# Kernel tuning notes

Hardware: AMD Instinct MI355X
Metric: run time of the kernel (lower is better)

Reference implementation:

```python
import jax, jax.numpy as jnp
import numpy as np

B, H = 1024, 1024
V_OUT, V_INP = 50000, 32000
SRC = 256


def setup_inputs() -> dict:
    key = jax.random.key(0)
    ks = jax.random.split(key, 8)
    x = jax.random.normal(ks[0], (B, H), dtype=jnp.float32)
    W = jax.random.normal(ks[1], (V_OUT, H), dtype=jnp.float32) * 0.02
    b = jax.random.normal(ks[2], (V_OUT,), dtype=jnp.float32) * 0.02
    attn_scores = jax.random.uniform(ks[3], (B, SRC), dtype=jnp.float32)
    ctx_ids = jax.random.randint(ks[4], (B, SRC), 0, V_INP)
    inp_to_act = jax.random.randint(ks[5], (V_INP,), 0, V_OUT)
    out_map = jax.random.randint(ks[6], (V_OUT,), 0, V_OUT)
    actionmask = jax.random.randint(ks[7], (B, V_OUT), 0, 2).astype(jnp.int32)
    return {"x": x, "W": W, "b": b, "attn_scores": attn_scores,
            "ctx_ids": ctx_ids, "inp_to_act": inp_to_act,
            "out_map": out_map, "actionmask": actionmask}


def reference(x, W, b, attn_scores, ctx_ids, inp_to_act, out_map, actionmask):
    # gen scores: dense projection to output vocab, then remap rare ids
    gen_scores = x @ W.T + b                      # [B, V_out]
    gen_scores = gen_scores[:, out_map]           # index_select along vocab

    # pointer distribution: scatter-add attention mass onto input vocab ids
    bsz = gen_scores.shape[0]
    inpdist = jnp.zeros((bsz, V_INP), dtype=gen_scores.dtype)
    inpdist = inpdist.at[jnp.arange(bsz)[:, None], ctx_ids].add(attn_scores)

    # map input-vocab mass onto output vocab ids (scatter/set)
    ptr_scores = jnp.zeros((bsz, V_OUT), dtype=gen_scores.dtype)
    ptr_scores = ptr_scores.at[:, inp_to_act].set(inpdist)

    out_scores = gen_scores + ptr_scores
    gen_masked = gen_scores + (-1e6) * actionmask.astype(gen_scores.dtype)
    out_probs = jax.nn.softmax(out_scores, axis=-1)
    return (out_probs, gen_masked)
```

## Files before the change

kernel.cpp:

```cpp
#include <hip/hip_runtime.h>
#include <hip/hip_bf16.h>

#define B_    1024
#define H_    1024
#define VOUT  50000
#define VINP  32000
#define SRC_  256

#define BM 128
#define BN 128
#define BKK 32

typedef __bf16 bf16x8 __attribute__((ext_vector_type(8)));
typedef __bf16 bf16x4 __attribute__((ext_vector_type(4)));
typedef float  f32x4  __attribute__((ext_vector_type(4)));

__global__ void init_kernel(int* __restrict__ src_inp,
                            float* __restrict__ rowsum)
{
    int i = blockIdx.x * blockDim.x + threadIdx.x;
    if (i < VOUT) src_inp[i] = -1;
    if (i < B_)  rowsum[i] = 0.0f;
}

__global__ void scat_max_kernel(const int* __restrict__ i2a, int* __restrict__ src_inp) {
    int v = blockIdx.x * blockDim.x + threadIdx.x;
    if (v < VINP) atomicMax(&src_inp[i2a[v]], v);
}

__global__ __launch_bounds__(256) void gemm_kernel(
    const float* __restrict__ x, const float* __restrict__ W,
    const float* __restrict__ bias, const int* __restrict__ out_map,
    const int* __restrict__ amask,
    float* __restrict__ out_scores, float* __restrict__ gen_masked,
    float* __restrict__ rowsum)
{
    __shared__ __bf16 As[BM * BKK];
    __shared__ __bf16 Bs[BN * BKK];

    const int id = (int)(blockIdx.x + (blockIdx.y << 3));
    const int g  = id >> 3;
    const int by = (id & 7) * 49 + (g >> 3);
    if (by >= 391) return;
    const int bx = g & 7;
    const int m0 = bx * BM;
    const int n0 = by * BN;

    const int t  = threadIdx.x;
    const int tr = t >> 3;
    const int tk = (t & 7) << 2;

    const float* xrow[4];
    const float* wrow[4];
    #pragma unroll
    for (int p = 0; p < 4; ++p) {
        int r = tr + p * 32;
        xrow[p] = x + (size_t)(m0 + r) * H_ + tk;
        int n = n0 + r; if (n >= VOUT) n = VOUT - 1;
        wrow[p] = W + (size_t)out_map[n] * H_ + tk;
    }

    f32x4 acc[4][4];
    #pragma unroll
    for (int i = 0; i < 4; ++i)
        #pragma unroll
        for (int j = 0; j < 4; ++j)
            acc[i][j] = (f32x4){0.f, 0.f, 0.f, 0.f};

    const int wv   = t >> 6;
    const int wm   = (wv >> 1) * 64;
    const int wn   = (wv & 1) * 64;
    const int lane = t & 63;
    const int quad = lane >> 4;
    const int lr   = lane & 15;

    float4 ar[4], br[4];
    #pragma unroll
    for (int p = 0; p < 4; ++p) {
        ar[p] = *(const float4*)(xrow[p]);
        br[p] = *(const float4*)(wrow[p]);
    }

    for (int k0 = 0; k0 < H_; k0 += BKK) {
        #pragma unroll
        for (int p = 0; p < 4; ++p) {
            int r = tr + p * 32;
            bf16x4 a4, b4;
            a4.x = (__bf16)ar[p].x; a4.y = (__bf16)ar[p].y; a4.z = (__bf16)ar[p].z; a4.w = (__bf16)ar[p].w;
            b4.x = (__bf16)br[p].x; b4.y = (__bf16)br[p].y; b4.z = (__bf16)br[p].z; b4.w = (__bf16)br[p].w;
            *(bf16x4*)(&As[r * BKK + tk]) = a4;
            *(bf16x4*)(&Bs[r * BKK + tk]) = b4;
        }
        __syncthreads();

        if (k0 + BKK < H_) {
            #pragma unroll
            for (int p = 0; p < 4; ++p) {
                ar[p] = *(const float4*)(xrow[p] + k0 + BKK);
                br[p] = *(const float4*)(wrow[p] + k0 + BKK);
            }
        }

        bf16x8 af[4], bfr[4];
        #pragma unroll
        for (int i = 0; i < 4; ++i) {
            af[i]  = *(const bf16x8*)(&As[(wm + i * 16 + lr) * BKK + quad * 8]);
            bfr[i] = *(const bf16x8*)(&Bs[(wn + i * 16 + lr) * BKK + quad * 8]);
        }
        #pragma unroll
        for (int mi = 0; mi < 4; ++mi)
            #pragma unroll
            for (int ni = 0; ni < 4; ++ni)
                acc[mi][ni] = __builtin_amdgcn_mfma_f32_16x16x32_bf16(bfr[ni], af[mi], acc[mi][ni], 0, 0, 0);
        __syncthreads();
    }

    #pragma unroll
    for (int mi = 0; mi < 4; ++mi) {
        const int m = m0 + wm + mi * 16 + lr;
        float psum = 0.0f;
        #pragma unroll
        for (int ni = 0; ni < 4; ++ni) {
            const int n = n0 + wn + ni * 16 + (quad << 2);
            if (n < VOUT) {
                const size_t off = (size_t)m * VOUT + n;
                float4 v;
                v.x = acc[mi][ni][0] + bias[out_map[n + 0]];
                v.y = acc[mi][ni][1] + bias[out_map[n + 1]];
                v.z = acc[mi][ni][2] + bias[out_map[n + 2]];
                v.w = acc[mi][ni][3] + bias[out_map[n + 3]];
                *(float4*)(out_scores + off) = v;
                const int4 am = *(const int4*)(amask + off);
                float4 gm;
                gm.x = v.x - 1000000.0f * (float)am.x;
                gm.y = v.y - 1000000.0f * (float)am.y;
                gm.z = v.z - 1000000.0f * (float)am.z;
                gm.w = v.w - 1000000.0f * (float)am.w;
                *(float4*)(gen_masked + off) = gm;
                psum += __expf(v.x) + __expf(v.y) + __expf(v.z) + __expf(v.w);
            }
        }
        psum += __shfl_xor(psum, 16, 64);
        psum += __shfl_xor(psum, 32, 64);
        if (quad == 0) atomicAdd(rowsum + m, psum);
    }
}

__global__ void ptr_scatter_kernel(const float* __restrict__ attn,
                                   const int* __restrict__ ctx,
                                   const int* __restrict__ i2a,
                                   const int* __restrict__ src_inp,
                                   float* __restrict__ out_scores,
                                   float* __restrict__ rowsum)
{
    int idx = blockIdx.x * blockDim.x + threadIdx.x;
    int i = idx >> 8;
    int v = ctx[idx];
    int o = i2a[v];
    if (src_inp[o] == v) {
        float a   = attn[idx];
        float old = atomicAdd(out_scores + (size_t)i * VOUT + o, a);
        atomicAdd(rowsum + i, __expf(old + a) - __expf(old));
    }
}

__global__ __launch_bounds__(256) void norm_kernel(float* __restrict__ probs,
                                                   const float* __restrict__ rowsum)
{
    const int row = blockIdx.x;
    const float inv = 1.0f / rowsum[row];
    float4* p4 = (float4*)(probs + (size_t)row * VOUT);
    const int base = blockIdx.y * 3125;
    for (int i = base + threadIdx.x; i < base + 3125; i += 256) {
        float4 v = p4[i];
        v.x = __expf(v.x) * inv;
        v.y = __expf(v.y) * inv;
        v.z = __expf(v.z) * inv;
        v.w = __expf(v.w) * inv;
        p4[i] = v;
    }
}

extern "C" void kernel_launch(void* const* d_in, const int* in_sizes, int n_in,
                              void* d_out, int out_size, void* d_ws, size_t ws_size,
                              hipStream_t stream)
{
    const float* x     = (const float*)d_in[0];
    const float* W     = (const float*)d_in[1];
    const float* b     = (const float*)d_in[2];
    const float* attn  = (const float*)d_in[3];
    const int*   ctx   = (const int*)d_in[4];
    const int*   i2a   = (const int*)d_in[5];
    const int*   omap  = (const int*)d_in[6];
    const int*   amask = (const int*)d_in[7];

    float* out_probs  = (float*)d_out;
    float* gen_masked = out_probs + (size_t)B_ * VOUT;

    int*   src_inp = (int*)d_ws;
    float* rowsum  = (float*)(src_inp + VOUT);

    init_kernel<<<(VOUT + 255) / 256, 256, 0, stream>>>(src_inp, rowsum);
    scat_max_kernel<<<(VINP + 255) / 256, 256, 0, stream>>>(i2a, src_inp);

    dim3 grid(B_ / BM, 392);
    gemm_kernel<<<grid, 256, 0, stream>>>(x, W, b, omap, amask,
                                          out_probs, gen_masked, rowsum);

    ptr_scatter_kernel<<<(B_ * SRC_) / 256, 256, 0, stream>>>(attn, ctx, i2a, src_inp,
                                                              out_probs, rowsum);

    norm_kernel<<<dim3(B_, 4), 256, 0, stream>>>(out_probs, rowsum);
}
```

Baseline: 1.170 ms.

## Double-buffer GEMM shared memory and XOR-swizzle LDS layout

The GEMM main loop now uses two LDS buffers and keeps two register prefetch sets, so global loads run two k-steps ahead. This removes one barrier per k-step. The LDS write and read addresses are XOR-swizzled by row to cut bank conflicts on the bf16x8 fragment reads. In exchange it doubles LDS use and adds register pressure from the extra prefetch set, which may lower occupancy.

```diff
diff --git a/kernel.cpp b/kernel.cpp
--- a/kernel.cpp
+++ b/kernel.cpp
@@ -35,8 +35,8 @@
     float* __restrict__ out_scores, float* __restrict__ gen_masked,
     float* __restrict__ rowsum)
 {
-    __shared__ __bf16 As[BM * BKK];
-    __shared__ __bf16 Bs[BN * BKK];
+    __shared__ __bf16 As[2][BM * BKK];
+    __shared__ __bf16 Bs[2][BN * BKK];
 
     const int id = (int)(blockIdx.x + (blockIdx.y << 3));
     const int g  = id >> 3;
@@ -48,16 +48,20 @@
 
     const int t  = threadIdx.x;
     const int tr = t >> 3;
-    const int tk = (t & 7) << 2;
+    const int u  = t & 7;
+    const int tk = u << 2;
 
     const float* xrow[4];
     const float* wrow[4];
+    int scol[4];
     #pragma unroll
     for (int p = 0; p < 4; ++p) {
         int r = tr + p * 32;
         xrow[p] = x + (size_t)(m0 + r) * H_ + tk;
         int n = n0 + r; if (n >= VOUT) n = VOUT - 1;
         wrow[p] = W + (size_t)out_map[n] * H_ + tk;
+        int gg = (r >> 1) & 3;
+        scol[p] = r * BKK + ((((u >> 1) ^ gg) << 3) | ((u & 1) << 2));
     }
 
     f32x4 acc[4][4];
@@ -74,45 +78,64 @@
     const int quad = lane >> 4;
     const int lr   = lane & 15;
 
-    float4 ar[4], br[4];
-    #pragma unroll
-    for (int p = 0; p < 4; ++p) {
-        ar[p] = *(const float4*)(xrow[p]);
-        br[p] = *(const float4*)(wrow[p]);
-    }
-
-    for (int k0 = 0; k0 < H_; k0 += BKK) {
+    auto stage = [&](int buf, const float4* a, const float4* b) {
         #pragma unroll
         for (int p = 0; p < 4; ++p) {
-            int r = tr + p * 32;
             bf16x4 a4, b4;
-            a4.x = (__bf16)ar[p].x; a4.y = (__bf16)ar[p].y; a4.z = (__bf16)ar[p].z; a4.w = (__bf16)ar[p].w;
-            b4.x = (__bf16)br[p].x; b4.y = (__bf16)br[p].y; b4.z = (__bf16)br[p].z; b4.w = (__bf16)br[p].w;
-            *(bf16x4*)(&As[r * BKK + tk]) = a4;
-            *(bf16x4*)(&Bs[r * BKK + tk]) = b4;
-        }
-        __syncthreads();
-
-        if (k0 + BKK < H_) {
-            #pragma unroll
-            for (int p = 0; p < 4; ++p) {
-                ar[p] = *(const float4*)(xrow[p] + k0 + BKK);
-                br[p] = *(const float4*)(wrow[p] + k0 + BKK);
-            }
-        }
-
+            a4.x = (__bf16)a[p].x; a4.y = (__bf16)a[p].y; a4.z = (__bf16)a[p].z; a4.w = (__bf16)a[p].w;
+            b4.x = (__bf16)b[p].x; b4.y = (__bf16)b[p].y; b4.z = (__bf16)b[p].z; b4.w = (__bf16)b[p].w;
+            *(bf16x4*)(&As[buf][scol[p]]) = a4;
+            *(bf16x4*)(&Bs[buf][scol[p]]) = b4;
+        }
+    };
+
+    auto compute = [&](int buf) {
         bf16x8 af[4], bfr[4];
         #pragma unroll
         for (int i = 0; i < 4; ++i) {
-            af[i]  = *(const bf16x8*)(&As[(wm + i * 16 + lr) * BKK + quad * 8]);
-            bfr[i] = *(const bf16x8*)(&Bs[(wn + i * 16 + lr) * BKK + quad * 8]);
+            int Ra = wm + i * 16 + lr;
+            int Rb = wn + i * 16 + lr;
+            af[i]  = *(const bf16x8*)(&As[buf][Ra * BKK + ((quad ^ ((Ra >> 1) & 3)) << 3)]);
+            bfr[i] = *(const bf16x8*)(&Bs[buf][Rb * BKK + ((quad ^ ((Rb >> 1) & 3)) << 3)]);
         }
         #pragma unroll
         for (int mi = 0; mi < 4; ++mi)
             #pragma unroll
             for (int ni = 0; ni < 4; ++ni)
                 acc[mi][ni] = __builtin_amdgcn_mfma_f32_16x16x32_bf16(bfr[ni], af[mi], acc[mi][ni], 0, 0, 0);
+    };
+
+    float4 a0[4], b0[4], a1[4], b1[4];
+    #pragma unroll
+    for (int p = 0; p < 4; ++p) {
+        a0[p] = *(const float4*)(xrow[p]);
+        b0[p] = *(const float4*)(wrow[p]);
+        a1[p] = *(const float4*)(xrow[p] + BKK);
+        b1[p] = *(const float4*)(wrow[p] + BKK);
+    }
+
+    for (int k0 = 0; k0 < H_; k0 += 2 * BKK) {
+        stage(0, a0, b0);
+        if (k0 + 2 * BKK < H_) {
+            #pragma unroll
+            for (int p = 0; p < 4; ++p) {
+                a0[p] = *(const float4*)(xrow[p] + k0 + 2 * BKK);
+                b0[p] = *(const float4*)(wrow[p] + k0 + 2 * BKK);
+            }
+        }
         __syncthreads();
+        compute(0);
+
+        stage(1, a1, b1);
+        if (k0 + 3 * BKK < H_) {
+            #pragma unroll
+            for (int p = 0; p < 4; ++p) {
+                a1[p] = *(const float4*)(xrow[p] + k0 + 3 * BKK);
+                b1[p] = *(const float4*)(wrow[p] + k0 + 3 * BKK);
+            }
+        }
+        __syncthreads();
+        compute(1);
     }
 
     #pragma unroll
```

New measurement: 1.141 ms. 1.03x faster.

## Pre-convert W and x to swizzled bf16 and stage via direct global-to-LDS loads

Applied to the files above, without the earlier changes.

Adds pre-pass kernels that gather W rows through out_map, convert W and x to bf16 in an XOR-swizzled layout, and precompute the remapped bias. The GEMM then uses global_load_lds with double-buffered LDS tiles instead of register fp32 loads plus in-loop conversion, which removes conversion work and the out_map indirection from the main loop and halves operand bytes. This adds a full extra pass over W (about 200MB read, 100MB written) and needs workspace; when workspace is small it borrows the gen_masked buffer and runs a separate mask kernel afterwards.

```diff
diff --git a/kernel.cpp b/kernel.cpp
--- a/kernel.cpp
+++ b/kernel.cpp
@@ -6,14 +6,21 @@
 #define VOUT  50000
 #define VINP  32000
 #define SRC_  256
+#define NPAD  50048
 
 #define BM 128
 #define BN 128
 #define BKK 32
+#define NSTEP (H_ / BKK)
 
 typedef __bf16 bf16x8 __attribute__((ext_vector_type(8)));
-typedef __bf16 bf16x4 __attribute__((ext_vector_type(4)));
 typedef float  f32x4  __attribute__((ext_vector_type(4)));
+
+__device__ __forceinline__ void ldsload16(const __bf16* g, __bf16* l) {
+    __builtin_amdgcn_global_load_lds(
+        (const __attribute__((address_space(1))) void*)g,
+        (__attribute__((address_space(3))) void*)l, 16, 0, 0);
+}
 
 __global__ void init_kernel(int* __restrict__ src_inp,
                             float* __restrict__ rowsum)
@@ -28,15 +35,58 @@
     if (v < VINP) atomicMax(&src_inp[i2a[v]], v);
 }
 
+__global__ __launch_bounds__(256) void conv_w(
+    const float* __restrict__ W, const int* __restrict__ omap,
+    const float* __restrict__ bias,
+    __bf16* __restrict__ wbf, float* __restrict__ bias_g)
+{
+    int idx = blockIdx.x * 256 + threadIdx.x;
+    int n   = idx >> 7;
+    int c7  = idx & 127;
+    bf16x8 v;
+    if (n < VOUT) {
+        int g = (n >> 1) & 3;
+        int chunk = c7 >> 2, w = c7 & 3;
+        const float* s = W + (size_t)omap[n] * H_ + chunk * 32 + ((w ^ g) << 3);
+        float4 f0 = *(const float4*)(s);
+        float4 f1 = *(const float4*)(s + 4);
+        v[0] = (__bf16)f0.x; v[1] = (__bf16)f0.y; v[2] = (__bf16)f0.z; v[3] = (__bf16)f0.w;
+        v[4] = (__bf16)f1.x; v[5] = (__bf16)f1.y; v[6] = (__bf16)f1.z; v[7] = (__bf16)f1.w;
+        if (c7 == 0) bias_g[n] = bias[omap[n]];
+    } else {
+        #pragma unroll
+        for (int e = 0; e < 8; ++e) v[e] = (__bf16)0.f;
+        if (c7 == 0) bias_g[n] = 0.f;
+    }
+    *(bf16x8*)(wbf + (size_t)idx * 8) = v;
+}
+
+__global__ __launch_bounds__(256) void conv_x(
+    const float* __restrict__ x, __bf16* __restrict__ xbf)
+{
+    int idx = blockIdx.x * 256 + threadIdx.x;
+    int m   = idx >> 7;
+    int c7  = idx & 127;
+    int g = (m >> 1) & 3;
+    int chunk = c7 >> 2, w = c7 & 3;
+    const float* s = x + (size_t)m * H_ + chunk * 32 + ((w ^ g) << 3);
+    float4 f0 = *(const float4*)(s);
+    float4 f1 = *(const float4*)(s + 4);
+    bf16x8 v;
+    v[0] = (__bf16)f0.x; v[1] = (__bf16)f0.y; v[2] = (__bf16)f0.z; v[3] = (__bf16)f0.w;
+    v[4] = (__bf16)f1.x; v[5] = (__bf16)f1.y; v[6] = (__bf16)f1.z; v[7] = (__bf16)f1.w;
+    *(bf16x8*)(xbf + (size_t)idx * 8) = v;
+}
+
+template<bool FUSED>
 __global__ __launch_bounds__(256) void gemm_kernel(
-    const float* __restrict__ x, const float* __restrict__ W,
-    const float* __restrict__ bias, const int* __restrict__ out_map,
-    const int* __restrict__ amask,
+    const __bf16* __restrict__ xbf, const __bf16* __restrict__ wbf,
+    const float* __restrict__ bias_g, const int* __restrict__ amask,
     float* __restrict__ out_scores, float* __restrict__ gen_masked,
     float* __restrict__ rowsum)
 {
-    __shared__ __bf16 As[BM * BKK];
-    __shared__ __bf16 Bs[BN * BKK];
+    __shared__ __bf16 As[2][BM * BKK];
+    __shared__ __bf16 Bs[2][BN * BKK];
 
     const int id = (int)(blockIdx.x + (blockIdx.y << 3));
     const int g  = id >> 3;
@@ -46,19 +96,25 @@
     const int m0 = bx * BM;
     const int n0 = by * BN;
 
-    const int t  = threadIdx.x;
-    const int tr = t >> 3;
-    const int tk = (t & 7) << 2;
-
-    const float* xrow[4];
-    const float* wrow[4];
-    #pragma unroll
-    for (int p = 0; p < 4; ++p) {
-        int r = tr + p * 32;
-        xrow[p] = x + (size_t)(m0 + r) * H_ + tk;
-        int n = n0 + r; if (n >= VOUT) n = VOUT - 1;
-        wrow[p] = W + (size_t)out_map[n] * H_ + tk;
-    }
+    const int t    = threadIdx.x;
+    const int wv   = t >> 6;
+    const int lane = t & 63;
+    const int quad = lane >> 4;
+    const int lr   = lane & 15;
+    const int wm   = (wv >> 1) * 64;
+    const int wn   = (wv & 1) * 64;
+
+    const __bf16* gA = xbf + (size_t)(m0 + wv * 16 + (lane >> 2)) * H_ + ((lane & 3) << 3);
+    const __bf16* gB = wbf + (size_t)(n0 + wv * 16 + (lane >> 2)) * H_ + ((lane & 3) << 3);
+
+    auto stage = [&](int buf, int k) {
+        __bf16* a = &As[0][0] + buf * (BM * BKK) + (wv * 16) * BKK;
+        __bf16* b = &Bs[0][0] + buf * (BN * BKK) + (wv * 16) * BKK;
+        ldsload16(gA + k,            a);
+        ldsload16(gA + 64 * H_ + k,  a + 64 * BKK);
+        ldsload16(gB + k,            b);
+        ldsload16(gB + 64 * H_ + k,  b + 64 * BKK);
+    };
 
     f32x4 acc[4][4];
     #pragma unroll
@@ -67,51 +123,30 @@
         for (int j = 0; j < 4; ++j)
             acc[i][j] = (f32x4){0.f, 0.f, 0.f, 0.f};
 
-    const int wv   = t >> 6;
-    const int wm   = (wv >> 1) * 64;
-    const int wn   = (wv & 1) * 64;
-    const int lane = t & 63;
-    const int quad = lane >> 4;
-    const int lr   = lane & 15;
-
-    float4 ar[4], br[4];
-    #pragma unroll
-    for (int p = 0; p < 4; ++p) {
-        ar[p] = *(const float4*)(xrow[p]);
-        br[p] = *(const float4*)(wrow[p]);
-    }
-
-    for (int k0 = 0; k0 < H_; k0 += BKK) {
-        #pragma unroll
-        for (int p = 0; p < 4; ++p) {
-            int r = tr + p * 32;
-            bf16x4 a4, b4;
-            a4.x = (__bf16)ar[p].x; a4.y = (__bf16)ar[p].y; a4.z = (__bf16)ar[p].z; a4.w = (__bf16)ar[p].w;
-            b4.x = (__bf16)br[p].x; b4.y = (__bf16)br[p].y; b4.z = (__bf16)br[p].z; b4.w = (__bf16)br[p].w;
-            *(bf16x4*)(&As[r * BKK + tk]) = a4;
-            *(bf16x4*)(&Bs[r * BKK + tk]) = b4;
-        }
-        __syncthreads();
-
-        if (k0 + BKK < H_) {
-            #pragma unroll
-            for (int p = 0; p < 4; ++p) {
-                ar[p] = *(const float4*)(xrow[p] + k0 + BKK);
-                br[p] = *(const float4*)(wrow[p] + k0 + BKK);
-            }
-        }
-
+    auto compute = [&](int buf) {
+        const __bf16* a  = &As[0][0] + buf * (BM * BKK);
+        const __bf16* bp = &Bs[0][0] + buf * (BN * BKK);
         bf16x8 af[4], bfr[4];
         #pragma unroll
         for (int i = 0; i < 4; ++i) {
-            af[i]  = *(const bf16x8*)(&As[(wm + i * 16 + lr) * BKK + quad * 8]);
-            bfr[i] = *(const bf16x8*)(&Bs[(wn + i * 16 + lr) * BKK + quad * 8]);
+            int Ra = wm + i * 16 + lr;
+            int Rb = wn + i * 16 + lr;
+            af[i]  = *(const bf16x8*)(a  + Ra * BKK + ((quad ^ ((Ra >> 1) & 3)) << 3));
+            bfr[i] = *(const bf16x8*)(bp + Rb * BKK + ((quad ^ ((Rb >> 1) & 3)) << 3));
         }
         #pragma unroll
         for (int mi = 0; mi < 4; ++mi)
             #pragma unroll
             for (int ni = 0; ni < 4; ++ni)
                 acc[mi][ni] = __builtin_amdgcn_mfma_f32_16x16x32_bf16(bfr[ni], af[mi], acc[mi][ni], 0, 0, 0);
+    };
+
+    stage(0, 0);
+    __syncthreads();
+    for (int ts = 0; ts < NSTEP; ++ts) {
+        int cur = ts & 1;
+        if (ts + 1 < NSTEP) stage(cur ^ 1, (ts + 1) * BKK);
+        compute(cur);
         __syncthreads();
     }
 
@@ -124,19 +159,22 @@
             const int n = n0 + wn + ni * 16 + (quad << 2);
             if (n < VOUT) {
                 const size_t off = (size_t)m * VOUT + n;
+                const float4 bb = *(const float4*)(bias_g + n);
                 float4 v;
-                v.x = acc[mi][ni][0] + bias[out_map[n + 0]];
-                v.y = acc[mi][ni][1] + bias[out_map[n + 1]];
-                v.z = acc[mi][ni][2] + bias[out_map[n + 2]];
-                v.w = acc[mi][ni][3] + bias[out_map[n + 3]];
+                v.x = acc[mi][ni][0] + bb.x;
+                v.y = acc[mi][ni][1] + bb.y;
+                v.z = acc[mi][ni][2] + bb.z;
+                v.w = acc[mi][ni][3] + bb.w;
                 *(float4*)(out_scores + off) = v;
-                const int4 am = *(const int4*)(amask + off);
-                float4 gm;
-                gm.x = v.x - 1000000.0f * (float)am.x;
-                gm.y = v.y - 1000000.0f * (float)am.y;
-                gm.z = v.z - 1000000.0f * (float)am.z;
-                gm.w = v.w - 1000000.0f * (float)am.w;
-                *(float4*)(gen_masked + off) = gm;
+                if (FUSED) {
+                    const int4 am = *(const int4*)(amask + off);
+                    float4 gm;
+                    gm.x = v.x - 1000000.0f * (float)am.x;
+                    gm.y = v.y - 1000000.0f * (float)am.y;
+                    gm.z = v.z - 1000000.0f * (float)am.z;
+                    gm.w = v.w - 1000000.0f * (float)am.w;
+                    *(float4*)(gen_masked + off) = gm;
+                }
                 psum += __expf(v.x) + __expf(v.y) + __expf(v.z) + __expf(v.w);
             }
         }
@@ -144,6 +182,21 @@
         psum += __shfl_xor(psum, 32, 64);
         if (quad == 0) atomicAdd(rowsum + m, psum);
     }
+}
+
+__global__ __launch_bounds__(256) void mask_kernel(
+    const float* __restrict__ scores, const int* __restrict__ amask,
+    float* __restrict__ gen)
+{
+    size_t i = (size_t)blockIdx.x * 256 + threadIdx.x;
+    const float4 s = ((const float4*)scores)[i];
+    const int4  a = ((const int4*)amask)[i];
+    float4 gm;
+    gm.x = s.x - 1000000.0f * (float)a.x;
+    gm.y = s.y - 1000000.0f * (float)a.y;
+    gm.z = s.z - 1000000.0f * (float)a.z;
+    gm.w = s.w - 1000000.0f * (float)a.w;
+    ((float4*)gen)[i] = gm;
 }
 
 __global__ void ptr_scatter_kernel(const float* __restrict__ attn,
@@ -200,12 +253,28 @@
     int*   src_inp = (int*)d_ws;
     float* rowsum  = (float*)(src_inp + VOUT);
 
+    const size_t scratch_bytes = (size_t)NPAD * H_ * 2 + (size_t)B_ * H_ * 2 + (size_t)NPAD * 4;
+    const size_t ws_need = (size_t)VOUT * 4 + (size_t)B_ * 4 + scratch_bytes;
+    const bool ws_big = ws_size >= ws_need + 1024;
+    char* scratch = ws_big ? (char*)(rowsum + B_) : (char*)gen_masked;
+    __bf16* wbf    = (__bf16*)scratch;
+    __bf16* xbf    = wbf + (size_t)NPAD * H_;
+    float*  bias_g = (float*)(xbf + (size_t)B_ * H_);
+
     init_kernel<<<(VOUT + 255) / 256, 256, 0, stream>>>(src_inp, rowsum);
     scat_max_kernel<<<(VINP + 255) / 256, 256, 0, stream>>>(i2a, src_inp);
+    conv_w<<<NPAD * 128 / 256, 256, 0, stream>>>(W, omap, b, wbf, bias_g);
+    conv_x<<<B_ * 128 / 256, 256, 0, stream>>>(x, xbf);
 
     dim3 grid(B_ / BM, 392);
-    gemm_kernel<<<grid, 256, 0, stream>>>(x, W, b, omap, amask,
-                                          out_probs, gen_masked, rowsum);
+    if (ws_big) {
+        gemm_kernel<true><<<grid, 256, 0, stream>>>(xbf, wbf, bias_g, amask,
+                                                    out_probs, gen_masked, rowsum);
+    } else {
+        gemm_kernel<false><<<grid, 256, 0, stream>>>(xbf, wbf, bias_g, nullptr,
+                                                     out_probs, nullptr, rowsum);
+        mask_kernel<<<B_ * VOUT / 4 / 256, 256, 0, stream>>>(out_probs, amask, gen_masked);
+    }
 
     ptr_scatter_kernel<<<(B_ * SRC_) / 256, 256, 0, stream>>>(attn, ctx, i2a, src_inp,
                                                               out_probs, rowsum);
```

Result: faster. 1.122 ms (-4.1%).
